# Kernel tuning notes

Hardware: AMD Instinct MI355X
Metric: run time of the kernel (lower is better)

## Reference

```python
import jax, jax.numpy as jnp
import numpy as np

CFG = {"dt": 1.0, "T_r": 2.0, "kappa_j": 1.0, "tau_j": 10.0, "gamma_m": 1.0, "R_m": 1.0,
       "tau_m": 20.0, "thresh": 1.0, "tau_tr": 20.0, "tau_data": 10.0,
       "alpha_gen": 0.5, "alpha_disc": 0.5}


def _lif(v, x, tr, j, refrac, ti, cfg):
    """One LIF update for a hidden layer (bPC_SNNLayer.update_state)."""
    dt = cfg["dt"]
    j = j + dt / cfg["tau_j"] * (-cfg["kappa_j"] * j + ti)
    is_refr = refrac > 0
    v_next = v + dt / cfg["tau_m"] * (-cfg["gamma_m"] * v + cfg["R_m"] * j)
    v = jnp.where(is_refr, v, v_next)
    spikes = (v > cfg["thresh"]).astype(v.dtype) * (1.0 - is_refr.astype(v.dtype))
    v = v * (1.0 - spikes)
    refrac = jnp.maximum(refrac - dt, 0.0)
    refrac = jnp.where(spikes > 0, jnp.asarray(cfg["T_r"], v.dtype), refrac)
    tr = tr - tr / cfg["tau_tr"] + spikes  # spike trace (layer.x)
    return v, spikes, tr, j, refrac


def _forward(x_data, y_target, W0, W1, W2, V0, V1, V2, num_steps):
    cfg = CFG
    B = x_data.shape[0]
    d0, d1, d2, d3 = x_data.shape[1], W0.shape[1], W1.shape[1], W2.shape[1]
    dt_ = x_data.dtype
    z = lambda d: jnp.zeros((B, d), dt_)
    state = dict(v1=z(d1), tr1=z(d1), j1=z(d1), r1=z(d1), s1=z(d1),
                 v2=z(d2), tr2=z(d2), j2=z(d2), r2=z(d2), s2=z(d2),
                 eg0=z(d0), eg1=z(d1), eg2=z(d2),
                 ed1=z(d1), ed2=z(d2), ed3=z(d3),
                 z_data=z(d0), z_label=z(d3))
    ag, ad = cfg["alpha_gen"], cfg["alpha_disc"]

    def step(st, _):
        # phase 1: currents into hidden layers 1 and 2 (layers 0/3 are data/label, no-op)
        ti1 = -st["eg1"] + st["ed2"] @ V1 - st["ed1"] + st["eg0"] @ W0
        ti2 = -st["eg2"] + st["ed3"] @ V2 - st["ed2"] + st["eg1"] @ W1
        v1, s1, tr1, j1, r1 = _lif(st["v1"], st["tr1"], st["tr1"], st["j1"], st["r1"], ti1, cfg) if False else _lif(st["v1"], st["tr1"], st["tr1"], st["j1"], st["r1"], ti1, cfg)
        v1, s1, tr1, j1, r1 = _lif(st["v1"], st["tr1"], st["tr1"], st["j1"], st["r1"], ti1, cfg)
        v2, s2, tr2, j2, r2 = _lif(st["v2"], st["tr2"], st["tr2"], st["j2"], st["r2"], ti2, cfg)
        # phase 2: error recomputation (training mode with label clamped)
        z_data = st["z_data"] - st["z_data"] / cfg["tau_data"] + x_data
        z_label = st["z_label"] - st["z_label"] / cfg["tau_data"] + y_target
        eg0 = ag * (z_data - s1 @ W0.T)          # layer 0 generative error
        ed1 = ad * (tr1 - x_data @ V0.T)          # layer 1 discriminative error
        eg1 = ag * (tr1 - s2 @ W1.T)
        ed2 = ad * (tr2 - s1 @ V1.T)
        eg2 = ag * (tr2 - y_target @ W2.T)        # top hidden: label-clamped generative target
        ed3 = ad * (z_label - s2 @ V2.T)          # label layer discriminative error
        return dict(v1=v1, tr1=tr1, j1=j1, r1=r1, s1=s1,
                    v2=v2, tr2=tr2, j2=j2, r2=r2, s2=s2,
                    eg0=eg0, eg1=eg1, eg2=eg2, ed1=ed1, ed2=ed2, ed3=ed3,
                    z_data=z_data, z_label=z_label), None

    final, _ = jax.lax.scan(step, state, None, length=num_steps)
    return final["ed3"]


def setup_inputs() -> dict:
    key = jax.random.key(0)
    ks = jax.random.split(key, 8)
    B = 128
    sizes = (2048, 4096, 4096, 512)
    sc = 0.02  # weight scale kept small so dynamics stay numerically sane over 16 steps
    return {
        "x_data": jax.random.normal(ks[0], (B, sizes[0]), jnp.float32),
        "y_target": jax.random.normal(ks[1], (B, sizes[3]), jnp.float32),
        "W0": jax.random.normal(ks[2], (sizes[0], sizes[1]), jnp.float32) * sc,
        "W1": jax.random.normal(ks[3], (sizes[1], sizes[2]), jnp.float32) * sc,
        "W2": jax.random.normal(ks[4], (sizes[2], sizes[3]), jnp.float32) * sc,
        "V0": jax.random.normal(ks[5], (sizes[1], sizes[0]), jnp.float32) * sc,
        "V1": jax.random.normal(ks[6], (sizes[2], sizes[1]), jnp.float32) * sc,
        "V2": jax.random.normal(ks[7], (sizes[3], sizes[2]), jnp.float32) * sc,
        "num_steps": 16,
    }


def reference(x_data, y_target, W0, W1, W2, V0, V1, V2, num_steps):
    return _forward(x_data, y_target, W0, W1, W2, V0, V1, V2, num_steps)
```

## Files before the change

kernel.cpp:

```cpp
#include <hip/hip_runtime.h>


#define DEVINL __device__ __forceinline__

using bf16x8 = __attribute__((ext_vector_type(8))) __bf16;
using f32x4  = __attribute__((ext_vector_type(4))) float;
using i32x4  = __attribute__((ext_vector_type(4))) int;
typedef unsigned char uchar;

static constexpr int BB = 128;
static constexpr int D0 = 2048, D1 = 4096, D2 = 4096, D3 = 512;
static constexpr int NSTEPS = 16;

struct Ctx {
  const float *x, *y, *W0, *W1, *W2, *V0, *V1, *V2;
  float *v1, *j1, *r1, *tr1, *v2, *j2, *r2, *tr2;
  float *zd, *zl, *xV0T, *yW2T;
  __bf16 *x_bf, *y_bf, *eg0_bf, *eg1_bf, *ed2_bf, *ed3_bf;
  uchar *s1_f8, *s2_f8, *WA8, *WB8;
  __bf16 *W0t, *W1t, *V1t, *V2t, *V0n, *W2n;
  float *out;
};

DEVINL void gload16(const void* g, void* l) {
  __builtin_amdgcn_global_load_lds(
      (const __attribute__((address_space(1))) void*)g,
      (__attribute__((address_space(3))) void*)l, 16, 0, 0);
}
DEVINL uint32_t lds_off(const void* p) {
  return (uint32_t)(uintptr_t)(__attribute__((address_space(3))) const void*)p;
}
DEVINL bf16x8 dsr128(uint32_t addr) {
  i32x4 r;
  asm volatile("ds_read_b128 %0, %1" : "=v"(r) : "v"(addr));
  return __builtin_bit_cast(bf16x8, r);
}
DEVINL long dsr64(uint32_t addr) {
  long r;
  asm volatile("ds_read_b64 %0, %1" : "=v"(r) : "v"(addr));
  return r;
}

struct Seg { const __bf16* A; unsigned ldA; const __bf16* W; unsigned ldW; int iters; };
struct SPtr { const __bf16 *a0, *a1, *w; };

DEVINL SPtr mkptr(const Seg& s, int t) {
  int r = t >> 3;
  int u = ((t & 7) ^ (r & 7)) * 8;
  SPtr p;
  p.a0 = s.A + (size_t)r * s.ldA + u;
  p.a1 = s.A + (size_t)(r + 32) * s.ldA + u;
  p.w  = s.W + (size_t)r * s.ldW + u;
  return p;
}

DEVINL void run_gemm(const Seg* segs, int nIter, __bf16* lsA, __bf16* lsW,
                     int t, int wm, int wn, int l16, int lg, f32x4* acc) {
  const int seg0it = segs[0].iters;
  SPtr p = mkptr(segs[0], t);
  int nxt = 0;
  auto stage = [&](int s) {
    __bf16* bA = lsA + (s & 3) * 4096;
    __bf16* bW = lsW + (s & 3) * 2048;
    gload16(p.a0, bA + t * 8);
    gload16(p.a1, bA + 2048 + t * 8);
    gload16(p.w,  bW + t * 8);
    p.a0 += 64; p.a1 += 64; p.w += 64;
    if (++nxt == seg0it) p = mkptr(segs[1], t);
  };

  const int x7 = l16 & 7;
  uint32_t aB = lds_off(lsA), wB = lds_off(lsW);
  uint32_t aAd[2][2], wAd[2];
#pragma unroll
  for (int mt = 0; mt < 2; ++mt)
#pragma unroll
    for (int ks = 0; ks < 2; ++ks)
      aAd[mt][ks] = aB + (uint32_t)(wm * 32 + mt * 16 + l16) * 128u
                       + (uint32_t)(((ks * 4 + lg) ^ x7) * 16);
#pragma unroll
  for (int ks = 0; ks < 2; ++ks)
    wAd[ks] = wB + (uint32_t)(wn * 16 + l16) * 128u
                 + (uint32_t)(((ks * 4 + lg) ^ x7) * 16);

  auto compute = [&](int i) {
    uint32_t oa = (uint32_t)(i & 3) * 8192u, ow = (uint32_t)(i & 3) * 4096u;
    bf16x8 a00 = dsr128(aAd[0][0] + oa);
    bf16x8 a01 = dsr128(aAd[0][1] + oa);
    bf16x8 a10 = dsr128(aAd[1][0] + oa);
    bf16x8 a11 = dsr128(aAd[1][1] + oa);
    bf16x8 b0  = dsr128(wAd[0] + ow);
    bf16x8 b1  = dsr128(wAd[1] + ow);
    asm volatile("s_waitcnt lgkmcnt(0)" ::: "memory");
    __builtin_amdgcn_sched_barrier(0);
    __builtin_amdgcn_s_setprio(1);
    acc[0] = __builtin_amdgcn_mfma_f32_16x16x32_bf16(a00, b0, acc[0], 0, 0, 0);
    acc[1] = __builtin_amdgcn_mfma_f32_16x16x32_bf16(a10, b0, acc[1], 0, 0, 0);
    acc[0] = __builtin_amdgcn_mfma_f32_16x16x32_bf16(a01, b1, acc[0], 0, 0, 0);
    acc[1] = __builtin_amdgcn_mfma_f32_16x16x32_bf16(a11, b1, acc[1], 0, 0, 0);
    __builtin_amdgcn_s_setprio(0);
  };

  stage(0); stage(1); stage(2);
  for (int i = 0; i < nIter - 3; ++i) {
    asm volatile("s_waitcnt vmcnt(6)" ::: "memory");
    __builtin_amdgcn_s_barrier();
    stage(i + 3);
    compute(i);
  }
  asm volatile("s_waitcnt vmcnt(6)" ::: "memory");
  __builtin_amdgcn_s_barrier();
  compute(nIter - 3);
  asm volatile("s_waitcnt vmcnt(3)" ::: "memory");
  __builtin_amdgcn_s_barrier();
  compute(nIter - 2);
  asm volatile("s_waitcnt vmcnt(0)" ::: "memory");
  __builtin_amdgcn_s_barrier();
  compute(nIter - 1);
}


__global__ __launch_bounds__(256, 2) void phase1_v7(Ctx c, float edsc) {
  __shared__ __align__(16) __bf16 lsA[4][4096];
  __shared__ __align__(16) __bf16 lsW[4][2048];
  int t = threadIdx.x, w = t >> 6, l = t & 63;
  int l16 = l & 15, lg = l >> 4, wm = w >> 1, wn = w & 1;
  int bx = blockIdx.x;
  int z = bx >> 8, idx = bx & 255;
  int mh = idx & 1, n0 = (idx >> 1) * 32;
  f32x4 acc[2];
  f32x4 z4 = {0.f, 0.f, 0.f, 0.f};
  acc[0] = z4; acc[1] = z4;

  Seg segs[2]; int nIter, N;
  float *v, *j, *rf, *tr; const float* aux; const __bf16* buf; uchar* sf8;
  if (z == 0) {
    segs[0] = { c.ed2_bf + (size_t)mh * 64 * D2, (unsigned)D2, c.V1t + (size_t)n0 * D2, (unsigned)D2, 64 };
    segs[1] = { c.eg0_bf + (size_t)mh * 64 * D0, (unsigned)D0, c.W0t + (size_t)n0 * D0, (unsigned)D0, 32 };
    nIter = 96; N = D1;
    v = c.v1; j = c.j1; rf = c.r1; tr = c.tr1; buf = c.eg1_bf; aux = c.xV0T; sf8 = c.s1_f8;
  } else {
    segs[0] = { c.ed3_bf + (size_t)mh * 64 * D3, (unsigned)D3, c.V2t + (size_t)n0 * D3, (unsigned)D3, 8 };
    segs[1] = { c.eg1_bf + (size_t)mh * 64 * D1, (unsigned)D1, c.W1t + (size_t)n0 * D1, (unsigned)D1, 64 };
    nIter = 72; N = D2;
    v = c.v2; j = c.j2; rf = c.r2; tr = c.tr2; buf = c.ed2_bf; aux = c.yW2T; sf8 = c.s2_f8;
  }

  run_gemm(segs, nIter, &lsA[0][0], &lsW[0][0], t, wm, wn, l16, lg, acc);

  int n = n0 + wn * 16 + l16;
#pragma unroll
  for (int mt = 0; mt < 2; ++mt) {
#pragma unroll
    for (int r = 0; r < 4; ++r) {
      int b = mh * 64 + wm * 32 + mt * 16 + lg * 4 + r;
      size_t idx2 = (size_t)b * N + n;
      float to = tr[idx2];
      float ti = acc[mt][r] - (float)buf[idx2] - edsc * (to - aux[idx2]);
      float jo = j[idx2];
      float jn = jo + 0.1f * (ti - jo);
      float ro = rf[idx2];
      float vo = v[idx2];
      bool refr = ro > 0.0f;
      float vn = refr ? vo : (vo + 0.05f * (jn - vo));
      float sp = (!refr && vn > 1.0f) ? 1.0f : 0.0f;
      if (sp != 0.0f) vn = 0.0f;
      float rn = fmaxf(ro - 1.0f, 0.0f);
      if (sp != 0.0f) rn = 2.0f;
      float tn = to - 0.05f * to + sp;
      v[idx2] = vn; j[idx2] = jn; rf[idx2] = rn; tr[idx2] = tn;
      sf8[idx2] = (sp != 0.0f) ? (uchar)0x38 : (uchar)0;
    }
  }
}


__global__ __launch_bounds__(256, 2) void phase2_v9(Ctx c) {
  __shared__ __align__(16) uchar lsA[8][4096];
  __shared__ __align__(16) uchar lsW[8][4096];
  int t = threadIdx.x, w = t >> 6, l = t & 63;
  int l16 = l & 15, lg = l >> 4, wm = w >> 1, wn = w & 1;
  int g = blockIdx.x, mh = blockIdx.y;

  const uchar *A, *W; int n0; bool isA;
  if (g < 96) { isA = true;  A = c.s1_f8 + (size_t)mh * 64 * D1; W = c.WA8 + (size_t)g * 64 * 4096;        n0 = g * 64; }
  else        { isA = false; A = c.s2_f8 + (size_t)mh * 64 * D2; W = c.WB8 + (size_t)(g - 96) * 64 * 4096; n0 = (g - 96) * 64; }

  f32x4 acc[4];
  f32x4 z4 = {0.f, 0.f, 0.f, 0.f};
#pragma unroll
  for (int i = 0; i < 4; i++) acc[i] = z4;

  int row = t >> 2, u = t & 3;
  int su = (u ^ ((row >> 1) & 3)) * 16;
  const uchar* pA = A + (size_t)row * 4096 + su;
  const uchar* pW = W + (size_t)row * 4096 + su;
  uchar* dA = &lsA[0][0] + t * 16;
  uchar* dW = &lsW[0][0] + t * 16;
  auto stage = [&](int s) {
    gload16(pA, dA + (s & 7) * 4096);
    gload16(pW, dW + (s & 7) * 4096);
    pA += 64; pW += 64;
  };

  uint32_t aB = lds_off(lsA), wB = lds_off(lsW);
  uint32_t adA[2][2], adW[2][2];
#pragma unroll
  for (int mt = 0; mt < 2; ++mt)
#pragma unroll
    for (int ks = 0; ks < 2; ++ks) {
      int ra = wm * 32 + mt * 16 + l16;
      adA[mt][ks] = aB + (uint32_t)ra * 64u
                  + (uint32_t)((((ks * 2 + (lg >> 1)) ^ ((ra >> 1) & 3)) * 16) + (lg & 1) * 8);
    }
#pragma unroll
  for (int nt = 0; nt < 2; ++nt)
#pragma unroll
    for (int ks = 0; ks < 2; ++ks) {
      int rw = wn * 32 + nt * 16 + l16;
      adW[nt][ks] = wB + (uint32_t)rw * 64u
                  + (uint32_t)((((ks * 2 + (lg >> 1)) ^ ((rw >> 1) & 3)) * 16) + (lg & 1) * 8);
    }

  auto compute = [&](int i) {
    uint32_t off = (uint32_t)(i & 7) * 4096u;
    long a0  = dsr64(adA[0][0] + off);
    long a1  = dsr64(adA[1][0] + off);
    long b0  = dsr64(adW[0][0] + off);
    long b1  = dsr64(adW[1][0] + off);
    long a0b = dsr64(adA[0][1] + off);
    long a1b = dsr64(adA[1][1] + off);
    long b0b = dsr64(adW[0][1] + off);
    long b1b = dsr64(adW[1][1] + off);
    asm volatile("s_waitcnt lgkmcnt(0)" ::: "memory");
    __builtin_amdgcn_sched_barrier(0);
    __builtin_amdgcn_s_setprio(1);
    acc[0] = __builtin_amdgcn_mfma_f32_16x16x32_fp8_fp8(a0,  b0,  acc[0], 0, 0, 0);
    acc[1] = __builtin_amdgcn_mfma_f32_16x16x32_fp8_fp8(a0,  b1,  acc[1], 0, 0, 0);
    acc[2] = __builtin_amdgcn_mfma_f32_16x16x32_fp8_fp8(a1,  b0,  acc[2], 0, 0, 0);
    acc[3] = __builtin_amdgcn_mfma_f32_16x16x32_fp8_fp8(a1,  b1,  acc[3], 0, 0, 0);
    acc[0] = __builtin_amdgcn_mfma_f32_16x16x32_fp8_fp8(a0b, b0b, acc[0], 0, 0, 0);
    acc[1] = __builtin_amdgcn_mfma_f32_16x16x32_fp8_fp8(a0b, b1b, acc[1], 0, 0, 0);
    acc[2] = __builtin_amdgcn_mfma_f32_16x16x32_fp8_fp8(a1b, b0b, acc[2], 0, 0, 0);
    acc[3] = __builtin_amdgcn_mfma_f32_16x16x32_fp8_fp8(a1b, b1b, acc[3], 0, 0, 0);
    __builtin_amdgcn_s_setprio(0);
  };

  const int nIter = 64;
  stage(0); stage(1); stage(2); stage(3); stage(4); stage(5);
  for (int i = 0; i < nIter - 6; ++i) {
    asm volatile("s_waitcnt vmcnt(10)" ::: "memory");
    __builtin_amdgcn_s_barrier();
    stage(i + 6);
    compute(i);
  }
  asm volatile("s_waitcnt vmcnt(10)" ::: "memory");
  __builtin_amdgcn_s_barrier();
  compute(nIter - 6);
  asm volatile("s_waitcnt vmcnt(8)" ::: "memory");
  __builtin_amdgcn_s_barrier();
  compute(nIter - 5);
  asm volatile("s_waitcnt vmcnt(6)" ::: "memory");
  __builtin_amdgcn_s_barrier();
  compute(nIter - 4);
  asm volatile("s_waitcnt vmcnt(4)" ::: "memory");
  __builtin_amdgcn_s_barrier();
  compute(nIter - 3);
  asm volatile("s_waitcnt vmcnt(2)" ::: "memory");
  __builtin_amdgcn_s_barrier();
  compute(nIter - 2);
  asm volatile("s_waitcnt vmcnt(0)" ::: "memory");
  __builtin_amdgcn_s_barrier();
  compute(nIter - 1);

#pragma unroll
  for (int mt = 0; mt < 2; ++mt)
#pragma unroll
    for (int nt = 0; nt < 2; ++nt) {
      int nn = n0 + wn * 32 + nt * 16 + l16;
#pragma unroll
      for (int r = 0; r < 4; ++r) {
        int b = mh * 64 + wm * 32 + mt * 16 + lg * 4 + r;
        float av = acc[mt * 2 + nt][r];
        if (isA) {
          if (nn < 2048) {
            size_t idx = (size_t)b * D0 + nn;
            float zo = c.zd[idx]; float zn = zo - 0.1f * zo + c.x[idx];
            c.zd[idx] = zn;
            c.eg0_bf[idx] = (__bf16)(0.5f * (zn - av));
          } else {
            size_t idx = (size_t)b * D2 + (nn - 2048);
            c.ed2_bf[idx] = (__bf16)(0.5f * (c.tr2[idx] - av));
          }
        } else {
          if (nn < 4096) {
            size_t idx = (size_t)b * D1 + nn;
            c.eg1_bf[idx] = (__bf16)(0.5f * (c.tr1[idx] - av));
          } else {
            size_t idx = (size_t)b * D3 + (nn - 4096);
            float zo = c.zl[idx]; float zn = zo - 0.1f * zo + c.y[idx];
            c.zl[idx] = zn;
            float e = 0.5f * (zn - av);
            c.out[idx] = e; c.ed3_bf[idx] = (__bf16)e;
          }
        }
      }
    }
}


__global__ __launch_bounds__(256, 2) void precomp_v6(Ctx c) {
  __shared__ __align__(16) __bf16 lsA[4][4096];
  __shared__ __align__(16) __bf16 lsW[4][2048];
  int t = threadIdx.x, w = t >> 6, l = t & 63;
  int l16 = l & 15, lg = l >> 4, wm = w >> 1, wn = w & 1;
  int n0 = blockIdx.x * 32, mh = blockIdx.y;
  f32x4 acc[2];
  f32x4 z4 = {0.f, 0.f, 0.f, 0.f};
  acc[0] = z4; acc[1] = z4;

  Seg segs[2]; int nIter, N; float* outp;
  if (blockIdx.z == 0) {
    segs[0] = { c.x_bf + (size_t)mh * 64 * D0, (unsigned)D0, c.V0n + (size_t)n0 * D0, (unsigned)D0, 32 };
    nIter = 32; N = D1; outp = c.xV0T;
  } else {
    segs[0] = { c.y_bf + (size_t)mh * 64 * D3, (unsigned)D3, c.W2n + (size_t)n0 * D3, (unsigned)D3, 8 };
    nIter = 8; N = D2; outp = c.yW2T;
  }
  segs[1] = segs[0];

  run_gemm(segs, nIter, &lsA[0][0], &lsW[0][0], t, wm, wn, l16, lg, acc);

  int n = n0 + wn * 16 + l16;
#pragma unroll
  for (int mt = 0; mt < 2; ++mt)
#pragma unroll
    for (int r = 0; r < 4; ++r) {
      int b = mh * 64 + wm * 32 + mt * 16 + lg * 4 + r;
      outp[(size_t)b * N + n] = acc[mt][r];
    }
}


__global__ __launch_bounds__(256) void wprep_kernel(Ctx c) {
  __shared__ float ls[64][65];
  int g = blockIdx.x;
  const float* src; __bf16* tp = nullptr; uchar* n8 = nullptr; __bf16* nb = nullptr; int R, C;
  if (g < 2048)       { src = c.W0; n8 = c.WA8;                         tp = c.W0t; R = D0; C = D1; }
  else if (g < 6144)  { g -= 2048;  src = c.W1; n8 = c.WB8;             tp = c.W1t; R = D1; C = D2; }
  else if (g < 10240) { g -= 6144;  src = c.V1; n8 = c.WA8 + (size_t)2048 * 4096; tp = c.V1t; R = D2; C = D1; }
  else if (g < 10752) { g -= 10240; src = c.V2; n8 = c.WB8 + (size_t)4096 * 4096; tp = c.V2t; R = D3; C = D2; }
  else if (g < 12800) { g -= 10752; src = c.V0; nb = c.V0n; R = D1; C = D0; }
  else                { g -= 12800; src = c.W2; nb = c.W2n; R = D2; C = D3; }
  int tpr = C / 64;
  int r0 = (g / tpr) * 64, c0 = (g % tpr) * 64;
  int t = threadIdx.x, r = t >> 2, q = t & 3;

  const float4* s4 = reinterpret_cast<const float4*>(src + (size_t)(r0 + r) * C + c0 + q * 16);
  if (n8) {
    int pk[4];
#pragma unroll
    for (int i = 0; i < 4; i++) {
      float4 v = s4[i];
      ls[r][q * 16 + i * 4 + 0] = v.x; ls[r][q * 16 + i * 4 + 1] = v.y;
      ls[r][q * 16 + i * 4 + 2] = v.z; ls[r][q * 16 + i * 4 + 3] = v.w;
      int wd = __builtin_amdgcn_cvt_pk_fp8_f32(v.x, v.y, 0, false);
      wd = __builtin_amdgcn_cvt_pk_fp8_f32(v.z, v.w, wd, true);
      pk[i] = wd;
    }
    int4 pv; pv.x = pk[0]; pv.y = pk[1]; pv.z = pk[2]; pv.w = pk[3];
    *reinterpret_cast<int4*>(n8 + (size_t)(r0 + r) * C + c0 + q * 16) = pv;
    __syncthreads();
    union { __bf16 h[16]; int4 qq[2]; } wv;
#pragma unroll
    for (int i = 0; i < 16; i++) wv.h[i] = (__bf16)ls[q * 16 + i][r];
    int4* dt = reinterpret_cast<int4*>(tp + (size_t)(c0 + r) * R + r0 + q * 16);
    dt[0] = wv.qq[0]; dt[1] = wv.qq[1];
  } else {
    union { __bf16 h[16]; int4 qq[2]; } uu;
#pragma unroll
    for (int i = 0; i < 4; i++) {
      float4 v = s4[i];
      uu.h[i * 4 + 0] = (__bf16)v.x; uu.h[i * 4 + 1] = (__bf16)v.y;
      uu.h[i * 4 + 2] = (__bf16)v.z; uu.h[i * 4 + 3] = (__bf16)v.w;
    }
    int4* dn = reinterpret_cast<int4*>(nb + (size_t)(r0 + r) * C + c0 + q * 16);
    dn[0] = uu.qq[0]; dn[1] = uu.qq[1];
  }
}

__global__ __launch_bounds__(256) void castinit_kernel(Ctx c) {
  int i = blockIdx.x * 256 + threadIdx.x;
  const int NX = BB * D0 / 4;
  union { __bf16 h[4]; uint2 u; } p, q;
  if (i < NX) {
    float4 xv = reinterpret_cast<const float4*>(c.x)[i];
    reinterpret_cast<float4*>(c.zd)[i] = xv;
    p.h[0] = (__bf16)xv.x; p.h[1] = (__bf16)xv.y; p.h[2] = (__bf16)xv.z; p.h[3] = (__bf16)xv.w;
    reinterpret_cast<uint2*>(c.x_bf)[i] = p.u;
    q.h[0] = (__bf16)(0.5f * xv.x); q.h[1] = (__bf16)(0.5f * xv.y);
    q.h[2] = (__bf16)(0.5f * xv.z); q.h[3] = (__bf16)(0.5f * xv.w);
    reinterpret_cast<uint2*>(c.eg0_bf)[i] = q.u;
  } else {
    int k = i - NX;
    float4 yv = reinterpret_cast<const float4*>(c.y)[k];
    reinterpret_cast<float4*>(c.zl)[k] = yv;
    p.h[0] = (__bf16)yv.x; p.h[1] = (__bf16)yv.y; p.h[2] = (__bf16)yv.z; p.h[3] = (__bf16)yv.w;
    reinterpret_cast<uint2*>(c.y_bf)[k] = p.u;
    q.h[0] = (__bf16)(0.5f * yv.x); q.h[1] = (__bf16)(0.5f * yv.y);
    q.h[2] = (__bf16)(0.5f * yv.z); q.h[3] = (__bf16)(0.5f * yv.w);
    reinterpret_cast<uint2*>(c.ed3_bf)[k] = q.u;
  }
}


extern "C" void kernel_launch(void* const* d_in, const int* in_sizes, int n_in,
                              void* d_out, int out_size, void* d_ws, size_t ws_size,
                              hipStream_t stream) {
  Ctx c;
  c.x  = (const float*)d_in[0];
  c.y  = (const float*)d_in[1];
  c.W0 = (const float*)d_in[2];
  c.W1 = (const float*)d_in[3];
  c.W2 = (const float*)d_in[4];
  c.V0 = (const float*)d_in[5];
  c.V1 = (const float*)d_in[6];
  c.V2 = (const float*)d_in[7];
  c.out = (float*)d_out;

  char* p = (char*)d_ws;
  auto af = [&](size_t n) -> float* { float* r = (float*)p; p += ((n * 4 + 255) & ~(size_t)255); return r; };
  auto ah = [&](size_t n) -> __bf16* { __bf16* r = (__bf16*)p; p += ((n * 2 + 255) & ~(size_t)255); return r; };
  auto au = [&](size_t n) -> uchar* { uchar* r = (uchar*)p; p += ((n + 255) & ~(size_t)255); return r; };

  const size_t S1 = (size_t)BB * D1;
  c.v1 = af(S1); c.j1 = af(S1); c.r1 = af(S1); c.tr1 = af(S1);
  c.v2 = af(S1); c.j2 = af(S1); c.r2 = af(S1); c.tr2 = af(S1);
  c.eg1_bf = ah(S1); c.ed2_bf = ah(S1);
  size_t zero_bytes = (size_t)(p - (char*)d_ws);
  c.zd = af((size_t)BB * D0); c.zl = af((size_t)BB * D3);
  c.xV0T = af(S1); c.yW2T = af(S1);
  c.x_bf = ah((size_t)BB * D0); c.y_bf = ah((size_t)BB * D3);
  c.eg0_bf = ah((size_t)BB * D0); c.ed3_bf = ah((size_t)BB * D3);
  c.s1_f8 = au(S1); c.s2_f8 = au(S1);
  c.W0t = ah((size_t)D0 * D1); c.W1t = ah((size_t)D1 * D2); c.V1t = ah((size_t)D2 * D1); c.V2t = ah((size_t)D3 * D2);
  c.V0n = ah((size_t)D1 * D0); c.W2n = ah((size_t)D2 * D3);
  c.WA8 = au((size_t)(D0 + D2) * 4096);
  c.WB8 = au((size_t)(D1 + D3) * 4096);

  hipMemsetAsync(d_ws, 0, zero_bytes, stream);
  castinit_kernel<<<320, 256, 0, stream>>>(c);
  wprep_kernel<<<13312, 256, 0, stream>>>(c);
  precomp_v6<<<dim3(128, 2, 2), 256, 0, stream>>>(c);

  for (int s = 1; s < NSTEPS; s++) {
    phase1_v7<<<512, 256, 0, stream>>>(c, 0.5f);
    phase2_v9<<<dim3(168, 2), 256, 0, stream>>>(c);
  }
}
```

Before: 947.2 us.

## Stage phase1 GEMM tiles through registers with a double-buffered LDS pipeline

Replaces the global_load_lds four-stage LDS pipeline in the phase1 GEMM with register-staged prefetch. Four tiles are held in registers and written to a two-buffer LDS ring, which halves the shared memory footprint. The weight prep launch is also split into four smaller launches by block-offset range. The aims are lower LDS use, possibly better occupancy, and more latency hiding from register prefetch, at the cost of extra VGPRs and more barriers.

```diff
diff --git a/kernel.cpp b/kernel.cpp
--- a/kernel.cpp
+++ b/kernel.cpp
@@ -39,6 +39,14 @@
   long r;
   asm volatile("ds_read_b64 %0, %1" : "=v"(r) : "v"(addr));
   return r;
+}
+DEVINL i32x4 greg16(const void* p) {
+  i32x4 r;
+  asm volatile("global_load_dwordx4 %0, %1, off" : "=v"(r) : "v"(p));
+  return r;
+}
+DEVINL void dsw128(uint32_t addr, i32x4 v) {
+  asm volatile("ds_write_b128 %0, %1" : : "v"(addr), "v"(v));
 }
 
 struct Seg { const __bf16* A; unsigned ldA; const __bf16* W; unsigned ldW; int iters; };
@@ -119,10 +127,91 @@
   compute(nIter - 1);
 }
 
-
-__global__ __launch_bounds__(256, 2) void phase1_v7(Ctx c, float edsc) {
-  __shared__ __align__(16) __bf16 lsA[4][4096];
-  __shared__ __align__(16) __bf16 lsW[4][2048];
+DEVINL void run_gemm_reg(const Seg* segs, int nIter, __bf16* lsA, __bf16* lsW,
+                         int t, int wm, int wn, int l16, int lg, f32x4* acc) {
+  const int seg0it = segs[0].iters;
+  SPtr p = mkptr(segs[0], t);
+  int nxt = 0;
+  auto advance = [&]() {
+    p.a0 += 64; p.a1 += 64; p.w += 64;
+    if (++nxt == seg0it) p = mkptr(segs[1], t);
+  };
+
+  uint32_t wa0 = lds_off(lsA) + (uint32_t)t * 16u;
+  uint32_t wa1 = wa0 + 4096u;
+  uint32_t ww  = lds_off(lsW) + (uint32_t)t * 16u;
+
+  const int x7 = l16 & 7;
+  uint32_t aB = lds_off(lsA), wB = lds_off(lsW);
+  uint32_t aAd[2][2], wAd[2];
+#pragma unroll
+  for (int mt = 0; mt < 2; ++mt)
+#pragma unroll
+    for (int ks = 0; ks < 2; ++ks)
+      aAd[mt][ks] = aB + (uint32_t)(wm * 32 + mt * 16 + l16) * 128u
+                       + (uint32_t)(((ks * 4 + lg) ^ x7) * 16);
+#pragma unroll
+  for (int ks = 0; ks < 2; ++ks)
+    wAd[ks] = wB + (uint32_t)(wn * 16 + l16) * 128u
+                 + (uint32_t)(((ks * 4 + lg) ^ x7) * 16);
+
+  auto compute2 = [&](uint32_t b) {
+    uint32_t oa = b * 8192u, ow = b * 4096u;
+    bf16x8 a00 = dsr128(aAd[0][0] + oa);
+    bf16x8 a01 = dsr128(aAd[0][1] + oa);
+    bf16x8 a10 = dsr128(aAd[1][0] + oa);
+    bf16x8 a11 = dsr128(aAd[1][1] + oa);
+    bf16x8 b0  = dsr128(wAd[0] + ow);
+    bf16x8 b1  = dsr128(wAd[1] + ow);
+    asm volatile("s_waitcnt lgkmcnt(0)" ::: "memory");
+    __builtin_amdgcn_sched_barrier(0);
+    __builtin_amdgcn_s_setprio(1);
+    acc[0] = __builtin_amdgcn_mfma_f32_16x16x32_bf16(a00, b0, acc[0], 0, 0, 0);
+    acc[1] = __builtin_amdgcn_mfma_f32_16x16x32_bf16(a10, b0, acc[1], 0, 0, 0);
+    acc[0] = __builtin_amdgcn_mfma_f32_16x16x32_bf16(a01, b1, acc[0], 0, 0, 0);
+    acc[1] = __builtin_amdgcn_mfma_f32_16x16x32_bf16(a11, b1, acc[1], 0, 0, 0);
+    __builtin_amdgcn_s_setprio(0);
+  };
+
+  i32x4 ra0[4], ra1[4], rw[4];
+#pragma unroll
+  for (int s = 0; s < 4; ++s) {
+    ra0[s] = greg16(p.a0); ra1[s] = greg16(p.a1); rw[s] = greg16(p.w);
+    advance();
+  }
+
+#define P1PHASE(S, DOLOAD, VMS)                                          \
+  {                                                                      \
+    asm volatile("s_waitcnt vmcnt(" VMS ")" ::: "memory");               \
+    dsw128(wa0 + (uint32_t)((S) & 1) * 8192u, ra0[S]);                   \
+    dsw128(wa1 + (uint32_t)((S) & 1) * 8192u, ra1[S]);                   \
+    dsw128(ww  + (uint32_t)((S) & 1) * 4096u, rw[S]);                    \
+    if (DOLOAD) {                                                        \
+      ra0[S] = greg16(p.a0); ra1[S] = greg16(p.a1); rw[S] = greg16(p.w); \
+      advance();                                                         \
+    }                                                                    \
+    asm volatile("s_waitcnt lgkmcnt(0)" ::: "memory");                   \
+    __builtin_amdgcn_s_barrier();                                        \
+    compute2((uint32_t)((S) & 1));                                       \
+  }
+
+  for (int i = 0; i <= nIter - 8; i += 4) {
+    P1PHASE(0, true, "9");
+    P1PHASE(1, true, "9");
+    P1PHASE(2, true, "9");
+    P1PHASE(3, true, "9");
+  }
+  P1PHASE(0, false, "9");
+  P1PHASE(1, false, "6");
+  P1PHASE(2, false, "3");
+  P1PHASE(3, false, "0");
+#undef P1PHASE
+}
+
+
+__global__ __launch_bounds__(256, 2) void phase1_v10(Ctx c, float edsc) {
+  __shared__ __align__(16) __bf16 lsA[2][4096];
+  __shared__ __align__(16) __bf16 lsW[2][2048];
   int t = threadIdx.x, w = t >> 6, l = t & 63;
   int l16 = l & 15, lg = l >> 4, wm = w >> 1, wn = w & 1;
   int bx = blockIdx.x;
@@ -146,7 +235,7 @@
     v = c.v2; j = c.j2; rf = c.r2; tr = c.tr2; buf = c.ed2_bf; aux = c.yW2T; sf8 = c.s2_f8;
   }
 
-  run_gemm(segs, nIter, &lsA[0][0], &lsW[0][0], t, wm, wn, l16, lg, acc);
+  run_gemm_reg(segs, nIter, &lsA[0][0], &lsW[0][0], t, wm, wn, l16, lg, acc);
 
   int n = n0 + wn * 16 + l16;
 #pragma unroll
@@ -342,9 +431,9 @@
 }
 
 
-__global__ __launch_bounds__(256) void wprep_kernel(Ctx c) {
+__global__ __launch_bounds__(256) void wprep_kernel(Ctx c, int g0) {
   __shared__ float ls[64][65];
-  int g = blockIdx.x;
+  int g = blockIdx.x + g0;
   const float* src; __bf16* tp = nullptr; uchar* n8 = nullptr; __bf16* nb = nullptr; int R, C;
   if (g < 2048)       { src = c.W0; n8 = c.WA8;                         tp = c.W0t; R = D0; C = D1; }
   else if (g < 6144)  { g -= 2048;  src = c.W1; n8 = c.WB8;             tp = c.W1t; R = D1; C = D2; }
@@ -450,11 +539,14 @@
 
   hipMemsetAsync(d_ws, 0, zero_bytes, stream);
   castinit_kernel<<<320, 256, 0, stream>>>(c);
-  wprep_kernel<<<13312, 256, 0, stream>>>(c);
+  wprep_kernel<<<2048, 256, 0, stream>>>(c, 0);
+  wprep_kernel<<<4096, 256, 0, stream>>>(c, 2048);
+  wprep_kernel<<<4096, 256, 0, stream>>>(c, 6144);
+  wprep_kernel<<<3072, 256, 0, stream>>>(c, 10240);
   precomp_v6<<<dim3(128, 2, 2), 256, 0, stream>>>(c);
 
   for (int s = 1; s < NSTEPS; s++) {
-    phase1_v7<<<512, 256, 0, stream>>>(c, 0.5f);
+    phase1_v10<<<512, 256, 0, stream>>>(c, 0.5f);
     phase2_v9<<<dim3(168, 2), 256, 0, stream>>>(c);
   }
 }
```

Measured after the change: 987.7 us. 4.3% more time.
